# Optimization experiments

Measured on AMD Instinct MI355X. Metric: run time of the kernel, lower is better.

The kernel has to match this reference:

```python
import jax, jax.numpy as jnp
import numpy as np

POOL_SIZE = 4
MAX_DIM = 256
GRID = MAX_DIM // POOL_SIZE  # 64
NUM_CELLS = GRID * GRID      # 4096
B = 64                        # static max_batch (batch.max()+1 in torch)
N = 1_000_000
C = 64


def setup_inputs() -> dict:
    key = jax.random.key(0)
    k1, k2, k3 = jax.random.split(key, 3)
    x = jax.random.normal(k1, (N, C), dtype=jnp.float32)
    pos = jax.random.randint(k2, (N, 2), 0, MAX_DIM, dtype=jnp.int64)
    batch = jnp.sort(jax.random.randint(k3, (N,), 0, B, dtype=jnp.int64))
    return {"x": x, "pos": pos, "batch": batch}


def reference(x, pos, batch):
    # voxel key: (batch, pos_x//pool, pos_y//pool) -> flat cell index
    qpos = pos[:, :2] // POOL_SIZE                       # [N, 2] int
    idx = batch * NUM_CELLS + qpos[:, 0] * GRID + qpos[:, 1]  # [N]
    num_seg = B * NUM_CELLS
    # scatter_reduce(amax, include_self=False): max over points in each cell
    pooled = jax.ops.segment_max(x, idx, num_segments=num_seg)  # empty -> -inf
    # cells with no points stay zero (output_x initialized to zeros in torch)
    counts = jax.ops.segment_sum(jnp.ones((x.shape[0], 1), x.dtype), idx,
                                 num_segments=num_seg)          # [num_seg, 1]
    pooled = jnp.where(counts > 0, pooled, jnp.zeros((), x.dtype))
    # [B, grid^2, C] -> flatten -> [B, grid^2 * C]
    return pooled.reshape(B, NUM_CELLS * x.shape[1])
```

## Files before the change

### kernel.cpp

```cpp
#include <hip/hip_runtime.h>

#define POOL_SHIFT 2
#define GRID_DIM 64
#define NUM_CELLS 4096
#define NCH 64
#define BATCH 64
#define NSEG (BATCH * NUM_CELLS)
#define NIL 0xFFFFFFFFu

__global__ __launch_bounds__(256) void build_lists(
    const int* __restrict__ pos, const int* __restrict__ batch,
    unsigned int* __restrict__ head, unsigned int* __restrict__ next, int n) {
    int p = blockIdx.x * blockDim.x + threadIdx.x;
    if (p >= n) return;
    int b  = batch[p];
    int px = pos[2 * p];
    int py = pos[2 * p + 1];
    int idx = b * NUM_CELLS + (px >> POOL_SHIFT) * GRID_DIM + (py >> POOL_SHIFT);
    unsigned int old = atomicExch(&head[idx], (unsigned int)p);
    next[p] = old;
}

__global__ __launch_bounds__(256) void gather_max(
    const float* __restrict__ x, const unsigned int* __restrict__ head,
    const unsigned int* __restrict__ next, float* __restrict__ out) {
    int wave = (int)((blockIdx.x * blockDim.x + threadIdx.x) >> 6);
    int lane = threadIdx.x & 63;
    if (wave >= NSEG) return;

    unsigned int p = head[wave];
    size_t obase = (size_t)wave * NCH + lane;
    if (p == NIL) {
        out[obase] = 0.0f;
        return;
    }
    float acc = -__builtin_inff();
    while (p != NIL) {
        unsigned int np = next[p];
        float v = x[(size_t)p * NCH + lane];
        acc = fmaxf(acc, v);
        p = np;
    }
    out[obase] = acc;
}

extern "C" void kernel_launch(void* const* d_in, const int* in_sizes, int n_in,
                              void* d_out, int out_size, void* d_ws, size_t ws_size,
                              hipStream_t stream) {
    const float* x   = (const float*)d_in[0];
    const int* pos   = (const int*)d_in[1];
    const int* batch = (const int*)d_in[2];
    float* out = (float*)d_out;

    int n = in_sizes[2];

    unsigned int* head = (unsigned int*)d_ws;
    unsigned int* next = head + NSEG;

    hipMemsetAsync(head, 0xFF, (size_t)NSEG * sizeof(unsigned int), stream);

    {
        int blocks = (n + 255) / 256;
        build_lists<<<blocks, 256, 0, stream>>>(pos, batch, head, next, n);
    }
    {
        int blocks = NSEG / 4;
        gather_max<<<blocks, 256, 0, stream>>>(x, head, next, out);
    }
}
```

Measured before the change: 456.4 us.

## Replace linked-list gather with counting-sort CSR and unrolled gather

```diff
diff --git a/kernel.cpp b/kernel.cpp
--- a/kernel.cpp
+++ b/kernel.cpp
@@ -6,40 +6,108 @@
 #define NCH 64
 #define BATCH 64
 #define NSEG (BATCH * NUM_CELLS)
-#define NIL 0xFFFFFFFFu
+#define SCAN_BLOCKS 1024
 
-__global__ __launch_bounds__(256) void build_lists(
-    const int* __restrict__ pos, const int* __restrict__ batch,
-    unsigned int* __restrict__ head, unsigned int* __restrict__ next, int n) {
-    int p = blockIdx.x * blockDim.x + threadIdx.x;
-    if (p >= n) return;
+__device__ __forceinline__ int cell_of(const int* __restrict__ pos,
+                                       const int* __restrict__ batch, int p) {
     int b  = batch[p];
     int px = pos[2 * p];
     int py = pos[2 * p + 1];
-    int idx = b * NUM_CELLS + (px >> POOL_SHIFT) * GRID_DIM + (py >> POOL_SHIFT);
-    unsigned int old = atomicExch(&head[idx], (unsigned int)p);
-    next[p] = old;
+    return b * NUM_CELLS + (px >> POOL_SHIFT) * GRID_DIM + (py >> POOL_SHIFT);
 }
 
-__global__ __launch_bounds__(256) void gather_max(
-    const float* __restrict__ x, const unsigned int* __restrict__ head,
-    const unsigned int* __restrict__ next, float* __restrict__ out) {
+__global__ __launch_bounds__(256) void count_kernel(
+    const int* __restrict__ pos, const int* __restrict__ batch,
+    unsigned int* __restrict__ counts, unsigned int* __restrict__ rank, int n) {
+    int p = blockIdx.x * blockDim.x + threadIdx.x;
+    if (p >= n) return;
+    int c = cell_of(pos, batch, p);
+    rank[p] = atomicAdd(&counts[c], 1u);
+}
+
+__global__ __launch_bounds__(256) void reduce_kernel(
+    const unsigned int* __restrict__ counts, unsigned int* __restrict__ blocksum) {
+    __shared__ unsigned int s[256];
+    int t = threadIdx.x;
+    s[t] = counts[blockIdx.x * 256 + t];
+    __syncthreads();
+    for (int off = 128; off > 0; off >>= 1) {
+        if (t < off) s[t] += s[t + off];
+        __syncthreads();
+    }
+    if (t == 0) blocksum[blockIdx.x] = s[0];
+}
+
+__global__ __launch_bounds__(1024) void scanblock_kernel(
+    const unsigned int* __restrict__ blocksum, unsigned int* __restrict__ blockbase) {
+    __shared__ unsigned int s[1024];
+    int t = threadIdx.x;
+    unsigned int own = blocksum[t];
+    s[t] = own;
+    __syncthreads();
+    for (int off = 1; off < 1024; off <<= 1) {
+        unsigned int v = (t >= off) ? s[t - off] : 0u;
+        __syncthreads();
+        s[t] += v;
+        __syncthreads();
+    }
+    blockbase[t] = s[t] - own;
+}
+
+__global__ __launch_bounds__(256) void offsets_kernel(
+    const unsigned int* __restrict__ counts, const unsigned int* __restrict__ blockbase,
+    unsigned int* __restrict__ offsets, int n) {
+    __shared__ unsigned int s[256];
+    int t = threadIdx.x, b = blockIdx.x;
+    unsigned int own = counts[b * 256 + t];
+    s[t] = own;
+    __syncthreads();
+    for (int off = 1; off < 256; off <<= 1) {
+        unsigned int v = (t >= off) ? s[t - off] : 0u;
+        __syncthreads();
+        s[t] += v;
+        __syncthreads();
+    }
+    unsigned int incl = s[t] + blockbase[b];
+    offsets[b * 256 + t] = incl - own;
+    if (b == SCAN_BLOCKS - 1 && t == 255) offsets[NSEG] = incl;
+}
+
+__global__ __launch_bounds__(256) void reorder_kernel(
+    const int* __restrict__ pos, const int* __restrict__ batch,
+    const unsigned int* __restrict__ rank, const unsigned int* __restrict__ offsets,
+    unsigned int* __restrict__ order, int n) {
+    int p = blockIdx.x * blockDim.x + threadIdx.x;
+    if (p >= n) return;
+    int c = cell_of(pos, batch, p);
+    order[offsets[c] + rank[p]] = (unsigned int)p;
+}
+
+__global__ __launch_bounds__(256) void gather_kernel(
+    const float* __restrict__ x, const unsigned int* __restrict__ offsets,
+    const unsigned int* __restrict__ order, float* __restrict__ out) {
     int wave = (int)((blockIdx.x * blockDim.x + threadIdx.x) >> 6);
     int lane = threadIdx.x & 63;
-    if (wave >= NSEG) return;
+    unsigned int s = (unsigned int)__builtin_amdgcn_readfirstlane((int)offsets[wave]);
+    unsigned int e = (unsigned int)__builtin_amdgcn_readfirstlane((int)offsets[wave + 1]);
 
-    unsigned int p = head[wave];
     size_t obase = (size_t)wave * NCH + lane;
-    if (p == NIL) {
-        out[obase] = 0.0f;
-        return;
+    if (s == e) { out[obase] = 0.0f; return; }
+
+    float acc = -__builtin_inff();
+    unsigned int i = s;
+    for (; i + 4 <= e; i += 4) {
+        unsigned int p0 = order[i], p1 = order[i + 1],
+                     p2 = order[i + 2], p3 = order[i + 3];
+        float v0 = x[(size_t)p0 * NCH + lane];
+        float v1 = x[(size_t)p1 * NCH + lane];
+        float v2 = x[(size_t)p2 * NCH + lane];
+        float v3 = x[(size_t)p3 * NCH + lane];
+        acc = fmaxf(acc, fmaxf(fmaxf(v0, v1), fmaxf(v2, v3)));
     }
-    float acc = -__builtin_inff();
-    while (p != NIL) {
-        unsigned int np = next[p];
-        float v = x[(size_t)p * NCH + lane];
-        acc = fmaxf(acc, v);
-        p = np;
+    for (; i < e; ++i) {
+        unsigned int p = order[i];
+        acc = fmaxf(acc, x[(size_t)p * NCH + lane]);
     }
     out[obase] = acc;
 }
@@ -51,20 +119,22 @@
     const int* pos   = (const int*)d_in[1];
     const int* batch = (const int*)d_in[2];
     float* out = (float*)d_out;
-
     int n = in_sizes[2];
 
-    unsigned int* head = (unsigned int*)d_ws;
-    unsigned int* next = head + NSEG;
+    unsigned int* counts    = (unsigned int*)d_ws;
+    unsigned int* offsets   = counts + NSEG;
+    unsigned int* blocksum  = offsets + NSEG + 1;
+    unsigned int* blockbase = blocksum + 1024;
+    unsigned int* rank      = blockbase + 1024;
+    unsigned int* order     = rank + n;
 
-    hipMemsetAsync(head, 0xFF, (size_t)NSEG * sizeof(unsigned int), stream);
+    hipMemsetAsync(counts, 0, (size_t)NSEG * sizeof(unsigned int), stream);
 
-    {
-        int blocks = (n + 255) / 256;
-        build_lists<<<blocks, 256, 0, stream>>>(pos, batch, head, next, n);
-    }
-    {
-        int blocks = NSEG / 4;
-        gather_max<<<blocks, 256, 0, stream>>>(x, head, next, out);
-    }
+    int pblocks = (n + 255) / 256;
+    count_kernel<<<pblocks, 256, 0, stream>>>(pos, batch, counts, rank, n);
+    reduce_kernel<<<SCAN_BLOCKS, 256, 0, stream>>>(counts, blocksum);
+    scanblock_kernel<<<1, 1024, 0, stream>>>(blocksum, blockbase);
+    offsets_kernel<<<SCAN_BLOCKS, 256, 0, stream>>>(counts, blockbase, offsets, n);
+    reorder_kernel<<<pblocks, 256, 0, stream>>>(pos, batch, rank, offsets, order, n);
+    gather_kernel<<<NSEG / 4, 256, 0, stream>>>(x, offsets, order, out);
 }
```

Measured after the change: 446.9 us. 2.1% less time.
